# Performance work log

Measured on AMD Instinct MI355X. Metric: run time of the kernel, lower is better.

The kernel has to match this reference:

```python
import jax, jax.numpy as jnp
import numpy as np

V, P, T = 30522, 1024, 2
D, H, F, L = 768, 12, 3072, 4
HD = D // H
EPS = 1e-12


def layer_norm(x, g, b):
    mu = jnp.mean(x, axis=-1, keepdims=True)
    var = jnp.mean((x - mu) ** 2, axis=-1, keepdims=True)
    return (x - mu) * jax.lax.rsqrt(var + EPS) * g + b


def setup_inputs() -> dict:
    key = jax.random.key(0)
    ks = iter(jax.random.split(key, 32))
    s = 0.02
    inp = {
        "x": jax.random.randint(next(ks), (4, 1024), 0, V, dtype=jnp.int32),
        "word_emb": jax.random.normal(next(ks), (V, D), jnp.float32) * s,
        "pos_emb": jax.random.normal(next(ks), (P, D), jnp.float32) * s,
        "type_emb": jax.random.normal(next(ks), (T, D), jnp.float32) * s,
        "emb_g": jnp.ones((D,), jnp.float32),
        "emb_b": jnp.zeros((D,), jnp.float32),
        "Wq": jax.random.normal(next(ks), (L, D, D), jnp.float32) * s,
        "bq": jnp.zeros((L, D), jnp.float32),
        "Wk": jax.random.normal(next(ks), (L, D, D), jnp.float32) * s,
        "bk": jnp.zeros((L, D), jnp.float32),
        "Wv": jax.random.normal(next(ks), (L, D, D), jnp.float32) * s,
        "bv": jnp.zeros((L, D), jnp.float32),
        "Wo": jax.random.normal(next(ks), (L, D, D), jnp.float32) * s,
        "bo": jnp.zeros((L, D), jnp.float32),
        "ln1_g": jnp.ones((L, D), jnp.float32),
        "ln1_b": jnp.zeros((L, D), jnp.float32),
        "W1": jax.random.normal(next(ks), (L, D, F), jnp.float32) * s,
        "b1": jnp.zeros((L, F), jnp.float32),
        "W2": jax.random.normal(next(ks), (L, F, D), jnp.float32) * s,
        "b2": jnp.zeros((L, D), jnp.float32),
        "ln2_g": jnp.ones((L, D), jnp.float32),
        "ln2_b": jnp.zeros((L, D), jnp.float32),
        "Wp": jax.random.normal(next(ks), (D, D), jnp.float32) * s,
        "bp": jnp.zeros((D,), jnp.float32),
    }
    return inp


def _bert_forward(x, word_emb, pos_emb, type_emb, emb_g, emb_b,
                  Wq, bq, Wk, bk, Wv, bv, Wo, bo, ln1_g, ln1_b,
                  W1, b1, W2, b2, ln2_g, ln2_b, Wp, bp):
    B, S = x.shape
    # Embeddings (token_type_ids are all zeros in the original forward)
    h = word_emb[x] + pos_emb[:S][None, :, :] + type_emb[0][None, None, :]
    h = layer_norm(h, emb_g, emb_b)

    scale = 1.0 / np.sqrt(HD).astype(np.float32)

    def step(h, p):
        (wq, bq_, wk, bk_, wv, bv_, wo, bo_, g1, b1_, w1, bi1, w2, bi2, g2, b2_) = p
        q = (h @ wq + bq_).reshape(B, S, H, HD)
        k = (h @ wk + bk_).reshape(B, S, H, HD)
        v = (h @ wv + bv_).reshape(B, S, H, HD)
        att = jnp.einsum("bqhd,bkhd->bhqk", q, k) * scale
        att = jax.nn.softmax(att, axis=-1)
        o = jnp.einsum("bhqk,bkhd->bqhd", att, v).reshape(B, S, D)
        # attention output: dense + residual + LN
        h = layer_norm(o @ wo + bo_ + h, g1, b1_)
        # FFN (note: original applies GELU twice and has NO residual here)
        inter = jax.nn.gelu(h @ w1 + bi1, approximate=False)
        h = layer_norm(jax.nn.gelu(inter @ w2 + bi2, approximate=False), g2, b2_)
        return h, None

    params = (Wq, bq, Wk, bk, Wv, bv, Wo, bo, ln1_g, ln1_b, W1, b1, W2, b2, ln2_g, ln2_b)
    h, _ = jax.lax.scan(step, h, params)
    # Pooler on final hidden states (loop in original overwrites output each iter)
    return jnp.tanh(h[:, 0] @ Wp + bp)


def reference(x, word_emb, pos_emb, type_emb, emb_g, emb_b,
              Wq, bq, Wk, bk, Wv, bv, Wo, bo, ln1_g, ln1_b,
              W1, b1, W2, b2, ln2_g, ln2_b, Wp, bp):
    return _bert_forward(x, word_emb, pos_emb, type_emb, emb_g, emb_b,
                         Wq, bq, Wk, bk, Wv, bv, Wo, bo, ln1_g, ln1_b,
                         W1, b1, W2, b2, ln2_g, ln2_b, Wp, bp)
```

## Files before the change

### kernel.cpp

```cpp
#include <hip/hip_runtime.h>
#include <math.h>

namespace {

constexpr int B  = 4;
constexpr int S  = 1024;
constexpr int D  = 768;
constexpr int H  = 12;
constexpr int HD = 64;
constexpr int F  = 3072;
constexpr int L  = 4;
constexpr int M  = B * S;
constexpr int NQKV = 3 * D;
constexpr int NQK = 2 * D;

typedef __attribute__((ext_vector_type(4))) float    f32x4;
typedef _Float16 f16x8 __attribute__((ext_vector_type(8)));
typedef __attribute__((ext_vector_type(8))) unsigned short u16x8;
typedef __attribute__((ext_vector_type(4))) unsigned short u16x4;

__device__ __forceinline__ unsigned short f2h_u(float f) {
    _Float16 h = (_Float16)f;
    return __builtin_bit_cast(unsigned short, h);
}
__device__ __forceinline__ float h2f(unsigned short u) {
    return (float)__builtin_bit_cast(_Float16, u);
}

__device__ __forceinline__ void gload16(const void* gptr, void* ldsptr) {
    __builtin_amdgcn_global_load_lds(
        (const __attribute__((address_space(1))) unsigned int*)gptr,
        (__attribute__((address_space(3))) unsigned int*)ldsptr,
        16, 0, 0);
}

__device__ __forceinline__ float wave_sum(float v) {
#pragma unroll
    for (int off = 32; off; off >>= 1) v += __shfl_xor(v, off, 64);
    return v;
}
__device__ __forceinline__ float block_sum256(float v, float* sm) {
    v = wave_sum(v);
    __syncthreads();
    if ((threadIdx.x & 63) == 0) sm[threadIdx.x >> 6] = v;
    __syncthreads();
    return sm[0] + sm[1] + sm[2] + sm[3];
}

__device__ __forceinline__ void transpose_tile(const float* __restrict__ src,
                                               unsigned short* __restrict__ dst,
                                               int R, int C) {
    __shared__ float tile[32][33];
    const int cb = blockIdx.x * 32, rb = blockIdx.y * 32;
    const int t = threadIdx.x;
    {
        const int r = t >> 3, cq = (t & 7) * 4;
        const float4 v = *(const float4*)&src[(size_t)(rb + r) * C + cb + cq];
        tile[r][cq + 0] = v.x; tile[r][cq + 1] = v.y;
        tile[r][cq + 2] = v.z; tile[r][cq + 3] = v.w;
    }
    __syncthreads();
    {
        const int dc = t >> 3, rq = (t & 7) * 4;
        u16x4 o;
#pragma unroll
        for (int j = 0; j < 4; ++j) o[j] = f2h_u(tile[rq + j][dc]);
        *(u16x4*)&dst[(size_t)(cb + dc) * R + rb + rq] = o;
    }
}

__global__ __launch_bounds__(256) void transpose_qkvo_kernel(
    const float* __restrict__ Wq, const float* __restrict__ Wk,
    const float* __restrict__ Wv, const float* __restrict__ Wo,
    unsigned short* __restrict__ Wqkv_t, unsigned short* __restrict__ Wo_t) {
    const int z = blockIdx.z;
    const int l = z >> 2, which = z & 3;
    const float* src = (which == 0 ? Wq : which == 1 ? Wk : which == 2 ? Wv : Wo)
                       + (size_t)l * D * D;
    unsigned short* dst = (which < 3)
        ? Wqkv_t + ((size_t)l * NQKV + which * D) * D
        : Wo_t + (size_t)l * D * D;
    transpose_tile(src, dst, D, D);
}

__global__ __launch_bounds__(256) void transpose_w_kernel(
    const float* __restrict__ src0, unsigned short* __restrict__ dst0, int R, int C) {
    const int l = blockIdx.z;
    transpose_tile(src0 + (size_t)l * R * C, dst0 + (size_t)l * R * C, R, C);
}

__global__ __launch_bounds__(256) void bias_concat_kernel(
    const float* __restrict__ bq, const float* __restrict__ bk,
    const float* __restrict__ bv, float* __restrict__ bqkv) {
    const int i = blockIdx.x * 256 + threadIdx.x;
    if (i >= L * NQKV) return;
    const int l = i / NQKV, j = i % NQKV;
    float v = (j < D) ? bq[l * D + j] : (j < 2 * D) ? bk[l * D + j - D] : bv[l * D + j - 2 * D];
    bqkv[i] = v;
}

__global__ __launch_bounds__(256) void embed_ln_kernel(
    const int* __restrict__ x, const float* __restrict__ we,
    const float* __restrict__ pe, const float* __restrict__ te,
    const float* __restrict__ g, const float* __restrict__ bb,
    float* __restrict__ hres, unsigned short* __restrict__ hh) {
    __shared__ float sm[4];
    const int row = blockIdx.x;
    const int s = row & (S - 1);
    const int tok = x[row];
    const int t = threadIdx.x;
    const bool act = t < 192;
    const int d = t * 4;
    float v[4] = {};
    if (act) {
        const float4 w = *(const float4*)&we[(size_t)tok * D + d];
        const float4 p = *(const float4*)&pe[(size_t)s * D + d];
        const float4 tt = *(const float4*)&te[d];
        v[0] = w.x + p.x + tt.x; v[1] = w.y + p.y + tt.y;
        v[2] = w.z + p.z + tt.z; v[3] = w.w + p.w + tt.w;
    }
    const float mu = block_sum256(v[0] + v[1] + v[2] + v[3], sm) * (1.0f / D);
    float lvar = 0.f;
    if (act) {
#pragma unroll
        for (int i = 0; i < 4; ++i) { float dv = v[i] - mu; lvar += dv * dv; }
    }
    const float var = block_sum256(lvar, sm) * (1.0f / D);
    const float inv = rsqrtf(var + 1e-12f);
    if (act) {
        const float4 g4 = *(const float4*)&g[d];
        const float4 b4 = *(const float4*)&bb[d];
        float o[4];
        o[0] = (v[0] - mu) * inv * g4.x + b4.x;
        o[1] = (v[1] - mu) * inv * g4.y + b4.y;
        o[2] = (v[2] - mu) * inv * g4.z + b4.z;
        o[3] = (v[3] - mu) * inv * g4.w + b4.w;
        *(float4*)&hres[(size_t)row * D + d] = make_float4(o[0], o[1], o[2], o[3]);
        u16x4 ob;
#pragma unroll
        for (int i = 0; i < 4; ++i) ob[i] = f2h_u(o[i]);
        *(u16x4*)&hh[(size_t)row * D + d] = ob;
    }
}

template <int NPA, int NPB, bool GELU_, bool HAS_RES>
__global__ __launch_bounds__(256) void ln_reduce_kernel(
    const unsigned short* __restrict__ pA,
    const unsigned short* __restrict__ pB,
    const float* __restrict__ bias,
    const float* __restrict__ res,
    const float* __restrict__ g, const float* __restrict__ bb,
    float* __restrict__ outres, unsigned short* __restrict__ outh) {
    __shared__ float sm[4];
    const int row = blockIdx.x;
    const int t = threadIdx.x;
    const bool act = t < 192;
    const int d = t * 4;
    float v[4] = {};
    if (act) {
        const float4 bi = *(const float4*)&bias[d];
        v[0] = bi.x; v[1] = bi.y; v[2] = bi.z; v[3] = bi.w;
#pragma unroll
        for (int pp = 0; pp < NPA; ++pp) {
            const u16x4 pu = *(const u16x4*)&pA[(size_t)pp * M * D + (size_t)row * D + d];
#pragma unroll
            for (int i = 0; i < 4; ++i) v[i] += h2f(pu[i]);
        }
#pragma unroll
        for (int pp = 0; pp < NPB; ++pp) {
            const u16x4 pu = *(const u16x4*)&pB[(size_t)pp * M * D + (size_t)row * D + d];
#pragma unroll
            for (int i = 0; i < 4; ++i) v[i] += h2f(pu[i]);
        }
        if (HAS_RES) {
            const float4 rv = *(const float4*)&res[(size_t)row * D + d];
            v[0] += rv.x; v[1] += rv.y; v[2] += rv.z; v[3] += rv.w;
        }
        if (GELU_) {
#pragma unroll
            for (int i = 0; i < 4; ++i)
                v[i] = 0.5f * v[i] * (1.0f + erff(v[i] * 0.70710678118654752f));
        }
    }
    const float mu = block_sum256(v[0] + v[1] + v[2] + v[3], sm) * (1.0f / D);
    float lvar = 0.f;
    if (act) {
#pragma unroll
        for (int i = 0; i < 4; ++i) { float dv = v[i] - mu; lvar += dv * dv; }
    }
    const float var = block_sum256(lvar, sm) * (1.0f / D);
    const float inv = rsqrtf(var + 1e-12f);
    if (act) {
        const float4 g4 = *(const float4*)&g[d];
        const float4 b4 = *(const float4*)&bb[d];
        float o[4];
        o[0] = (v[0] - mu) * inv * g4.x + b4.x;
        o[1] = (v[1] - mu) * inv * g4.y + b4.y;
        o[2] = (v[2] - mu) * inv * g4.z + b4.z;
        o[3] = (v[3] - mu) * inv * g4.w + b4.w;
        *(float4*)&outres[(size_t)row * D + d] = make_float4(o[0], o[1], o[2], o[3]);
        u16x4 ob;
#pragma unroll
        for (int i = 0; i < 4; ++i) ob[i] = f2h_u(o[i]);
        *(u16x4*)&outh[(size_t)row * D + d] = ob;
    }
}

#define GEMM_STAGE(buf, k0)                                                          \
    do {                                                                             \
        gload16(Ab + (size_t)(rowBase + r0) * LDA + (k0) + c0 * 8, &Asl[buf][ldsOff0]); \
        gload16(Ab + (size_t)(rowBase + r1) * LDA + (k0) + c1 * 8, &Asl[buf][ldsOff1]); \
        gload16(Bb + (size_t)(colBase + r0) * LDA + (k0) + c0 * 8, &Bsl[buf][ldsOff0]); \
        gload16(Bb + (size_t)(colBase + r1) * LDA + (k0) + c1 * 8, &Bsl[buf][ldsOff1]); \
    } while (0)

#define GEMM_BODY(A_, Bw_, LDA_, KLEN_)                                              \
    constexpr int BK = 32;                                                           \
    __shared__ unsigned short Asl[3][128 * BK];                                      \
    __shared__ unsigned short Bsl[3][128 * BK];                                      \
    const unsigned short* Ab = (A_);                                                 \
    const unsigned short* Bb = (Bw_);                                                \
    const int LDA = (LDA_);                                                          \
    const int t = threadIdx.x;                                                       \
    const int lane = t & 63;                                                         \
    const int wid = t >> 6;                                                          \
    const int lr = lane & 15;                                                        \
    const int kh = lane >> 4;                                                        \
    const int wrBase = (wid >> 1) * 64;                                              \
    const int wcBase = (wid & 1) * 64;                                               \
    const int nwg = gridDim.x * gridDim.y;                                           \
    const int flatid = blockIdx.y * gridDim.x + blockIdx.x;                          \
    const int swzid = (flatid & 7) * (nwg >> 3) + (flatid >> 3);                     \
    const int rowBase = (swzid / gridDim.x) * 128;                                   \
    const int colBase = (swzid % gridDim.x) * 128;                                   \
    f32x4 acc[4][4] = {};                                                            \
    const int r0 = t >> 2, c0 = (t & 3) ^ ((r0 >> 1) & 3);                           \
    const int s_hi = 256 + t;                                                        \
    const int r1 = s_hi >> 2, c1 = (s_hi & 3) ^ ((r1 >> 1) & 3);                     \
    const unsigned ldsOff0 = (unsigned)((t & 192) * 8);                              \
    const unsigned ldsOff1 = (unsigned)((256 + (t & 192)) * 8);                      \
    const int nt = (KLEN_) / BK;                                                     \
    GEMM_STAGE(0, 0);                                                                \
    GEMM_STAGE(1, BK);                                                               \
    int p = 0;                                                                       \
    for (int tt = 0; tt < nt; ++tt) {                                                \
        if (tt + 1 < nt) asm volatile("s_waitcnt vmcnt(4)" ::: "memory");            \
        else             asm volatile("s_waitcnt vmcnt(0)" ::: "memory");            \
        __builtin_amdgcn_s_barrier();                                                \
        __builtin_amdgcn_sched_barrier(0);                                           \
        if (tt + 2 < nt) {                                                           \
            int nb = p + 2; if (nb >= 3) nb -= 3;                                    \
            GEMM_STAGE(nb, (tt + 2) * BK);                                           \
        }                                                                            \
        f16x8 af[4], bfr[4];                                                         \
        _Pragma("unroll")                                                            \
        for (int mi = 0; mi < 4; ++mi) {                                             \
            const int ar = wrBase + mi * 16 + lr;                                    \
            const int ch = kh ^ ((ar >> 1) & 3);                                     \
            af[mi] = *(const f16x8*)&Asl[p][ar * BK + ch * 8];                       \
        }                                                                            \
        _Pragma("unroll")                                                            \
        for (int nj = 0; nj < 4; ++nj) {                                             \
            const int bc = wcBase + nj * 16 + lr;                                    \
            const int ch = kh ^ ((bc >> 1) & 3);                                     \
            bfr[nj] = *(const f16x8*)&Bsl[p][bc * BK + ch * 8];                      \
        }                                                                            \
        __builtin_amdgcn_s_setprio(1);                                               \
        _Pragma("unroll")                                                            \
        for (int mi = 0; mi < 4; ++mi)                                               \
            _Pragma("unroll")                                                        \
            for (int nj = 0; nj < 4; ++nj)                                           \
                acc[mi][nj] = __builtin_amdgcn_mfma_f32_16x16x32_f16(                \
                    af[mi], bfr[nj], acc[mi][nj], 0, 0, 0);                          \
        __builtin_amdgcn_s_setprio(0);                                               \
        p = (p == 2) ? 0 : p + 1;                                                    \
    }

template <int EPI, typename CT>
__global__ __launch_bounds__(256) void gemm_mfma_kernel(
    const unsigned short* __restrict__ A, const unsigned short* __restrict__ Bw,
    const float* __restrict__ bias, CT* __restrict__ C, int N, int K) {
    GEMM_BODY(A, Bw, K, K)
#pragma unroll
    for (int nj = 0; nj < 4; ++nj) {
        const int col = colBase + wcBase + nj * 16 + lr;
        const float bc = bias[col];
#pragma unroll
        for (int mi = 0; mi < 4; ++mi) {
            const int row = rowBase + wrBase + mi * 16 + kh * 4;
#pragma unroll
            for (int j = 0; j < 4; ++j) {
                float v = acc[mi][nj][j] + bc;
                if (EPI == 1) v = 0.5f * v * (1.0f + erff(v * 0.70710678118654752f));
                if constexpr (sizeof(CT) == 4) C[(size_t)(row + j) * N + col] = v;
                else                           C[(size_t)(row + j) * N + col] = f2h_u(v);
            }
        }
    }
}

__global__ __launch_bounds__(256) void gemm_splitk_kernel(
    const unsigned short* __restrict__ A, const unsigned short* __restrict__ Bw,
    unsigned short* __restrict__ CpA, unsigned short* __restrict__ CpB,
    int ZA, int N, int Kfull, int Kc) {
    const int z = blockIdx.z;
    GEMM_BODY(A + (size_t)z * Kc, Bw + (size_t)z * Kc, Kfull, Kc)
    unsigned short* Cp = (z < ZA) ? (CpA + (size_t)z * M * N)
                                  : (CpB + (size_t)(z - ZA) * M * N);
#pragma unroll
    for (int nj = 0; nj < 4; ++nj) {
        const int col = colBase + wcBase + nj * 16 + lr;
#pragma unroll
        for (int mi = 0; mi < 4; ++mi) {
            const int row = rowBase + wrBase + mi * 16 + kh * 4;
#pragma unroll
            for (int j = 0; j < 4; ++j)
                Cp[(size_t)(row + j) * N + col] = f2h_u(acc[mi][nj][j]);
        }
    }
}

__global__ __launch_bounds__(256) void gemm_qkv_kernel(
    const unsigned short* __restrict__ A, const unsigned short* __restrict__ Bw,
    const float* __restrict__ bias, unsigned short* __restrict__ qkout,
    unsigned short* __restrict__ vtout) {
    GEMM_BODY(A, Bw, D, D)
    const bool isV = (colBase >= NQK);
#pragma unroll
    for (int nj = 0; nj < 4; ++nj) {
        const int col = colBase + wcBase + nj * 16 + lr;
        const float bc = bias[col];
        if (!isV) {
#pragma unroll
            for (int mi = 0; mi < 4; ++mi) {
                const int row = rowBase + wrBase + mi * 16 + kh * 4;
#pragma unroll
                for (int j = 0; j < 4; ++j)
                    qkout[(size_t)(row + j) * NQK + col] = f2h_u(acc[mi][nj][j] + bc);
            }
        } else {
            const int dd = col - NQK;
            const int h2 = dd >> 6, d6 = dd & 63;
#pragma unroll
            for (int mi = 0; mi < 4; ++mi) {
                const int row = rowBase + wrBase + mi * 16 + kh * 4;
                const int b2 = row >> 10, s2 = row & 1023;
                u16x4 ov;
#pragma unroll
                for (int j = 0; j < 4; ++j) ov[j] = f2h_u(acc[mi][nj][j] + bc);
                *(u16x4*)&vtout[(((size_t)(b2 * H + h2)) * 64 + d6) * S + s2] = ov;
            }
        }
    }
}

__global__ __launch_bounds__(256) void attention_kernel(
    const unsigned short* __restrict__ qk,
    const unsigned short* __restrict__ vt,
    unsigned short* __restrict__ o) {
    __shared__ unsigned short Qs[64 * 64];
    __shared__ unsigned short Ks[2][64 * 64];
    __shared__ unsigned short Vt[2][64 * 64];
    __shared__ _Float16 Ps[4][16 * 64];

    const int t = threadIdx.x;
    const int nwg = gridDim.x;
    const int flatid = blockIdx.x;
    const int lin = (flatid & 7) * (nwg >> 3) + (flatid >> 3);
    const int qt = lin & 15;
    const int bh = lin >> 4;
    const int b = bh / H, hh = bh % H;
    const int w = t >> 6;
    const int lr = t & 15;
    const int kh = (t >> 4) & 3;

    const int r0 = t >> 3;
    const int g0 = (t & 7) ^ (r0 & 7);
    const unsigned lo0 = (unsigned)((t & 192) * 8);
    const unsigned lo1 = (unsigned)(2048 + (t & 192) * 8);

    const unsigned short* kgb = qk + D + hh * HD;
    const unsigned short* vgb = vt + (size_t)bh * 64 * S;

    {
        const size_t qrow0 = (size_t)(b * S + qt * 64);
        gload16(qk + (qrow0 + r0) * NQK + hh * HD + g0 * 8, &Qs[lo0]);
        gload16(qk + (qrow0 + r0 + 32) * NQK + hh * HD + g0 * 8, &Qs[lo1]);
        gload16(kgb + (size_t)(b * S + r0) * NQK + g0 * 8, &Ks[0][lo0]);
        gload16(kgb + (size_t)(b * S + r0 + 32) * NQK + g0 * 8, &Ks[0][lo1]);
        gload16(vgb + (size_t)r0 * S + g0 * 8, &Vt[0][lo0]);
        gload16(vgb + (size_t)(r0 + 32) * S + g0 * 8, &Vt[0][lo1]);
    }
    __syncthreads();

    float m_[4] = {-INFINITY, -INFINITY, -INFINITY, -INFINITY};
    float l_[4] = {};
    f32x4 oacc[4] = {};
    const int swlo = (kh)     ^ (lr & 7);
    const int swhi = (kh + 4) ^ (lr & 7);
    constexpr int NT = S / 64;

    for (int it = 0; it < NT; ++it) {
        const int cur = it & 1;
        if (it + 1 < NT) {
            const int kt = (it + 1) * 64;
            gload16(kgb + (size_t)(b * S + kt + r0) * NQK + g0 * 8, &Ks[cur ^ 1][lo0]);
            gload16(kgb + (size_t)(b * S + kt + r0 + 32) * NQK + g0 * 8, &Ks[cur ^ 1][lo1]);
            gload16(vgb + (size_t)r0 * S + kt + g0 * 8, &Vt[cur ^ 1][lo0]);
            gload16(vgb + (size_t)(r0 + 32) * S + kt + g0 * 8, &Vt[cur ^ 1][lo1]);
        }

        const int qr = w * 16 + lr;
        f16x8 aq0 = *(const f16x8*)&Qs[qr * 64 + swlo * 8];
        f16x8 aq1 = *(const f16x8*)&Qs[qr * 64 + swhi * 8];
        f32x4 sc[4];
        __builtin_amdgcn_s_setprio(1);
#pragma unroll
        for (int nj = 0; nj < 4; ++nj) {
            const int kr = nj * 16 + lr;
            f16x8 b0 = *(const f16x8*)&Ks[cur][kr * 64 + swlo * 8];
            f16x8 b1 = *(const f16x8*)&Ks[cur][kr * 64 + swhi * 8];
            f32x4 z = {};
            z = __builtin_amdgcn_mfma_f32_16x16x32_f16(aq0, b0, z, 0, 0, 0);
            z = __builtin_amdgcn_mfma_f32_16x16x32_f16(aq1, b1, z, 0, 0, 0);
            sc[nj] = z;
        }
        __builtin_amdgcn_s_setprio(0);

        float alpha[4];
#pragma unroll
        for (int j = 0; j < 4; ++j) {
            float rm = fmaxf(fmaxf(sc[0][j], sc[1][j]), fmaxf(sc[2][j], sc[3][j])) * 0.125f;
#pragma unroll
            for (int off = 1; off < 16; off <<= 1) rm = fmaxf(rm, __shfl_xor(rm, off, 64));
            const float mn = fmaxf(m_[j], rm);
            alpha[j] = __expf(m_[j] - mn);
            m_[j] = mn;
        }
        float ph[4][4];
        float rs[4] = {};
#pragma unroll
        for (int nj = 0; nj < 4; ++nj)
#pragma unroll
            for (int j = 0; j < 4; ++j) {
                float p2 = __expf(fmaf(sc[nj][j], 0.125f, -m_[j]));
                ph[nj][j] = p2;
                rs[j] += p2;
            }
#pragma unroll
        for (int j = 0; j < 4; ++j) {
#pragma unroll
            for (int off = 1; off < 16; off <<= 1) rs[j] += __shfl_xor(rs[j], off, 64);
            l_[j] = l_[j] * alpha[j] + rs[j];
        }
        _Float16* psw = &Ps[w][0];
#pragma unroll
        for (int nj = 0; nj < 4; ++nj)
#pragma unroll
            for (int j = 0; j < 4; ++j) {
                const int pr = kh * 4 + j;
                const int pc = nj * 16 + lr;
                psw[pr * 64 + (((pc >> 3) ^ (pr & 7)) * 8) + (pc & 7)] = (_Float16)ph[nj][j];
            }
#pragma unroll
        for (int nj = 0; nj < 4; ++nj)
#pragma unroll
            for (int j = 0; j < 4; ++j) oacc[nj][j] *= alpha[j];

        f16x8 pa0 = *(const f16x8*)&psw[lr * 64 + swlo * 8];
        f16x8 pa1 = *(const f16x8*)&psw[lr * 64 + swhi * 8];
        __builtin_amdgcn_s_setprio(1);
#pragma unroll
        for (int nj = 0; nj < 4; ++nj) {
            const int vr = nj * 16 + lr;
            f16x8 b0 = *(const f16x8*)&Vt[cur][vr * 64 + swlo * 8];
            f16x8 b1 = *(const f16x8*)&Vt[cur][vr * 64 + swhi * 8];
            oacc[nj] = __builtin_amdgcn_mfma_f32_16x16x32_f16(pa0, b0, oacc[nj], 0, 0, 0);
            oacc[nj] = __builtin_amdgcn_mfma_f32_16x16x32_f16(pa1, b1, oacc[nj], 0, 0, 0);
        }
        __builtin_amdgcn_s_setprio(0);

        __syncthreads();
    }

    float inv[4];
#pragma unroll
    for (int j = 0; j < 4; ++j) inv[j] = 1.0f / l_[j];
#pragma unroll
    for (int nj = 0; nj < 4; ++nj)
#pragma unroll
        for (int j = 0; j < 4; ++j) {
            const int token = b * S + qt * 64 + w * 16 + kh * 4 + j;
            o[(size_t)token * D + hh * HD + nj * 16 + lr] = f2h_u(oacc[nj][j] * inv[j]);
        }
}

__global__ __launch_bounds__(768) void pooler_partial_kernel(
    const float* __restrict__ h, const float* __restrict__ Wp,
    float* __restrict__ partial) {
    const int slice = blockIdx.x;
    const int b = blockIdx.y;
    const int d = threadIdx.x;
    const float* hrow = h + (size_t)b * S * D + slice * 48;
    const float* wcol = Wp + (size_t)slice * 48 * D + d;
    float acc = 0.f;
#pragma unroll
    for (int kk = 0; kk < 48; ++kk) acc = fmaf(hrow[kk], wcol[(size_t)kk * D], acc);
    partial[((size_t)b * 16 + slice) * D + d] = acc;
}

__global__ __launch_bounds__(768) void pooler_reduce_kernel(
    const float* __restrict__ partial, const float* __restrict__ bp,
    float* __restrict__ out) {
    const int b = blockIdx.x;
    const int d = threadIdx.x;
    float acc = bp[d];
#pragma unroll
    for (int s2 = 0; s2 < 16; ++s2) acc += partial[((size_t)b * 16 + s2) * D + d];
    out[(size_t)b * D + d] = tanhf(acc);
}

}

extern "C" void kernel_launch(void* const* d_in, const int* in_sizes, int n_in,
                              void* d_out, int out_size, void* d_ws, size_t ws_size,
                              hipStream_t stream) {
    (void)in_sizes; (void)n_in; (void)out_size; (void)ws_size;

    const int*   x     = (const int*)  d_in[0];
    const float* we    = (const float*)d_in[1];
    const float* pe    = (const float*)d_in[2];
    const float* te    = (const float*)d_in[3];
    const float* emb_g = (const float*)d_in[4];
    const float* emb_b = (const float*)d_in[5];
    const float* Wq    = (const float*)d_in[6];
    const float* bq    = (const float*)d_in[7];
    const float* Wk    = (const float*)d_in[8];
    const float* bk    = (const float*)d_in[9];
    const float* Wv    = (const float*)d_in[10];
    const float* bv    = (const float*)d_in[11];
    const float* Wo    = (const float*)d_in[12];
    const float* bo    = (const float*)d_in[13];
    const float* ln1_g = (const float*)d_in[14];
    const float* ln1_b = (const float*)d_in[15];
    const float* W1    = (const float*)d_in[16];
    const float* b1    = (const float*)d_in[17];
    const float* W2    = (const float*)d_in[18];
    const float* b2    = (const float*)d_in[19];
    const float* ln2_g = (const float*)d_in[20];
    const float* ln2_b = (const float*)d_in[21];
    const float* Wp    = (const float*)d_in[22];
    const float* bp    = (const float*)d_in[23];

    char* wp8 = (char*)d_ws;
    float*          h_res  = (float*)wp8;              wp8 += (size_t)M * D * 4;
    unsigned short* h_f16  = (unsigned short*)wp8;     wp8 += (size_t)M * D * 2;
    unsigned short* blockA = (unsigned short*)wp8;     wp8 += (size_t)M * F * 2;
    unsigned short* qk_f   = blockA;
    unsigned short* v_t    = blockA + (size_t)M * NQK;
    unsigned short* attno  = v_t + (size_t)B * H * 64 * S;
    unsigned short* inter  = blockA;
    unsigned short* wo_part = blockA;
    char*           oproj8 = wp8;                      wp8 += (size_t)M * D * 4;
    unsigned short* f2_part = (unsigned short*)oproj8;
    unsigned short* Wqkv_t = (unsigned short*)wp8;     wp8 += (size_t)L * NQKV * D * 2;
    unsigned short* Wo_t   = (unsigned short*)wp8;     wp8 += (size_t)L * D * D * 2;
    unsigned short* W1_t   = (unsigned short*)wp8;     wp8 += (size_t)L * F * D * 2;
    unsigned short* W2_t   = (unsigned short*)wp8;     wp8 += (size_t)L * D * F * 2;
    float*          bqkv   = (float*)wp8;              wp8 += (size_t)L * NQKV * 4;
    float*          ppart  = (float*)wp8;

    transpose_qkvo_kernel<<<dim3(24, 24, 16), 256, 0, stream>>>(Wq, Wk, Wv, Wo, Wqkv_t, Wo_t);
    transpose_w_kernel<<<dim3(96, 24, 4), 256, 0, stream>>>(W1, W1_t, D, F);
    transpose_w_kernel<<<dim3(24, 96, 4), 256, 0, stream>>>(W2, W2_t, F, D);
    bias_concat_kernel<<<dim3((L * NQKV + 255) / 256), 256, 0, stream>>>(bq, bk, bv, bqkv);

    embed_ln_kernel<<<M, 256, 0, stream>>>(x, we, pe, te, emb_g, emb_b, h_res, h_f16);

    for (int l = 0; l < L; ++l) {
        gemm_qkv_kernel<<<dim3(NQKV / 128, M / 128), 256, 0, stream>>>(
            h_f16, Wqkv_t + (size_t)l * NQKV * D, bqkv + l * NQKV, qk_f, v_t);

        attention_kernel<<<(S / 64) * B * H, 256, 0, stream>>>(qk_f, v_t, attno);

        gemm_splitk_kernel<<<dim3(D / 128, M / 128, 3), 256, 0, stream>>>(
            attno, Wo_t + (size_t)l * D * D, wo_part, nullptr, 3, D, D, 256);
        ln_reduce_kernel<3, 0, false, true><<<M, 256, 0, stream>>>(
            wo_part, nullptr, bo + l * D, h_res, ln1_g + l * D, ln1_b + l * D, h_res, h_f16);

        gemm_mfma_kernel<1, unsigned short><<<dim3(F / 128, M / 128), 256, 0, stream>>>(
            h_f16, W1_t + (size_t)l * F * D, b1 + l * F, inter, F, D);

        gemm_splitk_kernel<<<dim3(D / 128, M / 128, 3), 256, 0, stream>>>(
            inter, W2_t + (size_t)l * D * F, f2_part, h_f16, 2, D, F, 1024);
        ln_reduce_kernel<2, 1, true, false><<<M, 256, 0, stream>>>(
            f2_part, h_f16, b2 + l * D, nullptr, ln2_g + l * D, ln2_b + l * D, h_res, h_f16);
    }

    pooler_partial_kernel<<<dim3(16, B), 768, 0, stream>>>(h_res, Wp, ppart);
    pooler_reduce_kernel<<<B, 768, 0, stream>>>(ppart, bp, (float*)d_out);
}
```

Before: 720.5 us.

## Use double-buffered GEMM for main kernels and lazy softmax rescaling in attention

The plain GEMM and QKV GEMM now use a two-stage LDS pipeline instead of three, which cuts shared memory per block and may allow more resident blocks, at the cost of less prefetch depth. The split-K GEMM keeps the three-stage pipeline. The flash-attention loop skips the running-max update and accumulator rescaling unless a row max grows by more than 8 (a wave-wide vote). This trades exp and multiply work for fp16 probabilities that can reach up to e^8 before rescaling.

```diff
diff --git a/kernel.cpp b/kernel.cpp
--- a/kernel.cpp
+++ b/kernel.cpp
@@ -214,13 +214,7 @@
         gload16(Bb + (size_t)(colBase + r1) * LDA + (k0) + c1 * 8, &Bsl[buf][ldsOff1]); \
     } while (0)
 
-#define GEMM_BODY(A_, Bw_, LDA_, KLEN_)                                              \
-    constexpr int BK = 32;                                                           \
-    __shared__ unsigned short Asl[3][128 * BK];                                      \
-    __shared__ unsigned short Bsl[3][128 * BK];                                      \
-    const unsigned short* Ab = (A_);                                                 \
-    const unsigned short* Bb = (Bw_);                                                \
-    const int LDA = (LDA_);                                                          \
+#define GEMM_COMMON_IDS                                                              \
     const int t = threadIdx.x;                                                       \
     const int lane = t & 63;                                                         \
     const int wid = t >> 6;                                                          \
@@ -238,20 +232,10 @@
     const int s_hi = 256 + t;                                                        \
     const int r1 = s_hi >> 2, c1 = (s_hi & 3) ^ ((r1 >> 1) & 3);                     \
     const unsigned ldsOff0 = (unsigned)((t & 192) * 8);                              \
-    const unsigned ldsOff1 = (unsigned)((256 + (t & 192)) * 8);                      \
-    const int nt = (KLEN_) / BK;                                                     \
-    GEMM_STAGE(0, 0);                                                                \
-    GEMM_STAGE(1, BK);                                                               \
-    int p = 0;                                                                       \
-    for (int tt = 0; tt < nt; ++tt) {                                                \
-        if (tt + 1 < nt) asm volatile("s_waitcnt vmcnt(4)" ::: "memory");            \
-        else             asm volatile("s_waitcnt vmcnt(0)" ::: "memory");            \
-        __builtin_amdgcn_s_barrier();                                                \
-        __builtin_amdgcn_sched_barrier(0);                                           \
-        if (tt + 2 < nt) {                                                           \
-            int nb = p + 2; if (nb >= 3) nb -= 3;                                    \
-            GEMM_STAGE(nb, (tt + 2) * BK);                                           \
-        }                                                                            \
+    const unsigned ldsOff1 = (unsigned)((256 + (t & 192)) * 8);
+
+#define GEMM_READ_MFMA(p)                                                            \
+    {                                                                                \
         f16x8 af[4], bfr[4];                                                         \
         _Pragma("unroll")                                                            \
         for (int mi = 0; mi < 4; ++mi) {                                             \
@@ -273,6 +257,49 @@
                 acc[mi][nj] = __builtin_amdgcn_mfma_f32_16x16x32_f16(                \
                     af[mi], bfr[nj], acc[mi][nj], 0, 0, 0);                          \
         __builtin_amdgcn_s_setprio(0);                                               \
+    }
+
+#define GEMM_BODY2(A_, Bw_, LDA_, KLEN_)                                             \
+    constexpr int BK = 32;                                                           \
+    __shared__ unsigned short Asl[2][128 * BK];                                      \
+    __shared__ unsigned short Bsl[2][128 * BK];                                      \
+    const unsigned short* Ab = (A_);                                                 \
+    const unsigned short* Bb = (Bw_);                                                \
+    const int LDA = (LDA_);                                                          \
+    GEMM_COMMON_IDS                                                                  \
+    const int nt = (KLEN_) / BK;                                                     \
+    GEMM_STAGE(0, 0);                                                                \
+    for (int tt = 0; tt < nt; ++tt) {                                                \
+        const int p = tt & 1;                                                        \
+        asm volatile("s_waitcnt vmcnt(0)" ::: "memory");                             \
+        __builtin_amdgcn_s_barrier();                                                \
+        __builtin_amdgcn_sched_barrier(0);                                           \
+        if (tt + 1 < nt) { GEMM_STAGE(p ^ 1, (tt + 1) * BK); }                       \
+        GEMM_READ_MFMA(p)                                                            \
+    }
+
+#define GEMM_BODY3(A_, Bw_, LDA_, KLEN_)                                             \
+    constexpr int BK = 32;                                                           \
+    __shared__ unsigned short Asl[3][128 * BK];                                      \
+    __shared__ unsigned short Bsl[3][128 * BK];                                      \
+    const unsigned short* Ab = (A_);                                                 \
+    const unsigned short* Bb = (Bw_);                                                \
+    const int LDA = (LDA_);                                                          \
+    GEMM_COMMON_IDS                                                                  \
+    const int nt = (KLEN_) / BK;                                                     \
+    GEMM_STAGE(0, 0);                                                                \
+    GEMM_STAGE(1, BK);                                                               \
+    int p = 0;                                                                       \
+    for (int tt = 0; tt < nt; ++tt) {                                                \
+        if (tt + 1 < nt) asm volatile("s_waitcnt vmcnt(4)" ::: "memory");            \
+        else             asm volatile("s_waitcnt vmcnt(0)" ::: "memory");            \
+        __builtin_amdgcn_s_barrier();                                                \
+        __builtin_amdgcn_sched_barrier(0);                                           \
+        if (tt + 2 < nt) {                                                           \
+            int nb = p + 2; if (nb >= 3) nb -= 3;                                    \
+            GEMM_STAGE(nb, (tt + 2) * BK);                                           \
+        }                                                                            \
+        GEMM_READ_MFMA(p)                                                            \
         p = (p == 2) ? 0 : p + 1;                                                    \
     }
 
@@ -280,7 +307,7 @@
 __global__ __launch_bounds__(256) void gemm_mfma_kernel(
     const unsigned short* __restrict__ A, const unsigned short* __restrict__ Bw,
     const float* __restrict__ bias, CT* __restrict__ C, int N, int K) {
-    GEMM_BODY(A, Bw, K, K)
+    GEMM_BODY2(A, Bw, K, K)
 #pragma unroll
     for (int nj = 0; nj < 4; ++nj) {
         const int col = colBase + wcBase + nj * 16 + lr;
@@ -304,7 +331,7 @@
     unsigned short* __restrict__ CpA, unsigned short* __restrict__ CpB,
     int ZA, int N, int Kfull, int Kc) {
     const int z = blockIdx.z;
-    GEMM_BODY(A + (size_t)z * Kc, Bw + (size_t)z * Kc, Kfull, Kc)
+    GEMM_BODY3(A + (size_t)z * Kc, Bw + (size_t)z * Kc, Kfull, Kc)
     unsigned short* Cp = (z < ZA) ? (CpA + (size_t)z * M * N)
                                   : (CpB + (size_t)(z - ZA) * M * N);
 #pragma unroll
@@ -324,7 +351,7 @@
     const unsigned short* __restrict__ A, const unsigned short* __restrict__ Bw,
     const float* __restrict__ bias, unsigned short* __restrict__ qkout,
     unsigned short* __restrict__ vtout) {
-    GEMM_BODY(A, Bw, D, D)
+    GEMM_BODY2(A, Bw, D, D)
     const bool isV = (colBase >= NQK);
 #pragma unroll
     for (int nj = 0; nj < 4; ++nj) {
@@ -427,15 +454,25 @@
         }
         __builtin_amdgcn_s_setprio(0);
 
-        float alpha[4];
+        float rm_[4];
+        bool over = false;
 #pragma unroll
         for (int j = 0; j < 4; ++j) {
             float rm = fmaxf(fmaxf(sc[0][j], sc[1][j]), fmaxf(sc[2][j], sc[3][j])) * 0.125f;
 #pragma unroll
             for (int off = 1; off < 16; off <<= 1) rm = fmaxf(rm, __shfl_xor(rm, off, 64));
-            const float mn = fmaxf(m_[j], rm);
-            alpha[j] = __expf(m_[j] - mn);
-            m_[j] = mn;
+            rm_[j] = rm;
+            over = over || (rm > m_[j] + 8.0f);
+        }
+        const bool needR = __any(over);
+        float alpha[4] = {1.f, 1.f, 1.f, 1.f};
+        if (needR) {
+#pragma unroll
+            for (int j = 0; j < 4; ++j) {
+                const float mn = fmaxf(m_[j], rm_[j]);
+                alpha[j] = __expf(m_[j] - mn);
+                m_[j] = mn;
+            }
         }
         float ph[4][4];
         float rs[4] = {};
@@ -462,10 +499,12 @@
                 const int pc = nj * 16 + lr;
                 psw[pr * 64 + (((pc >> 3) ^ (pr & 7)) * 8) + (pc & 7)] = (_Float16)ph[nj][j];
             }
-#pragma unroll
-        for (int nj = 0; nj < 4; ++nj)
-#pragma unroll
-            for (int j = 0; j < 4; ++j) oacc[nj][j] *= alpha[j];
+        if (needR) {
+#pragma unroll
+            for (int nj = 0; nj < 4; ++nj)
+#pragma unroll
+                for (int j = 0; j < 4; ++j) oacc[nj][j] *= alpha[j];
+        }
 
         f16x8 pa0 = *(const f16x8*)&psw[lr * 64 + swlo * 8];
         f16x8 pa1 = *(const f16x8*)&psw[lr * 64 + swhi * 8];
```

Result: no change. 728.5 us (+1.1%).
